# Optimization experiments

Hardware: AMD Instinct MI355X
Metric: run time of the kernel (lower is better)

## Reference

```python
import jax, jax.numpy as jnp
import numpy as np

B, L, E, HL, HS, V, NC = 64, 512, 512, 1024, 256, 32000, 5
TAU = 1.0


def setup_inputs() -> dict:
    key = jax.random.key(0)
    ks = jax.random.split(key, 17)
    def p(k, shape, s=0.08):
        return jax.random.normal(k, shape, dtype=jnp.float32) * s
    eps = 1e-6
    return {
        "x": jax.random.randint(ks[0], (B, L), 0, V, dtype=jnp.int32),
        "gumbel_u": jax.random.uniform(ks[1], (B, L, 2), dtype=jnp.float32, minval=eps, maxval=1.0 - eps),
        "embedding": p(ks[2], (V, E), 0.1),
        "W_ih_l": p(ks[3], (4 * HL, E)),
        "W_hh_l": p(ks[4], (4 * HL, HL)),
        "b_ih_l": p(ks[5], (4 * HL,)),
        "b_hh_l": p(ks[6], (4 * HL,)),
        "W_ih_s": p(ks[7], (4 * HS, E)),
        "W_hh_s": p(ks[8], (4 * HS, HS)),
        "b_ih_s": p(ks[9], (4 * HS,)),
        "b_hh_s": p(ks[10], (4 * HS,)),
        "W_p": p(ks[11], (2, E + 2 * HL)),
        "b_p": p(ks[12], (2,)),
        "W_c1": p(ks[13], (512, HL)),
        "b_c1": p(ks[14], (512,)),
        "W_c2": p(ks[15], (NC, 512)),
        "b_c2": p(ks[16], (NC,)),
    }


def _lstm_cell(x, h, c, Wih, Whh, bih, bhh):
    # torch.nn.LSTMCell gate order: i, f, g, o
    gates = x @ Wih.T + bih + h @ Whh.T + bhh
    i, f, g, o = jnp.split(gates, 4, axis=-1)
    c2 = jax.nn.sigmoid(f) * c + jax.nn.sigmoid(i) * jnp.tanh(g)
    h2 = jax.nn.sigmoid(o) * jnp.tanh(c2)
    return h2, c2


def _forward(x, gumbel_u, embedding, W_ih_l, W_hh_l, b_ih_l, b_hh_l,
             W_ih_s, W_hh_s, b_ih_s, b_hh_s, W_p, b_p, W_c1, b_c1, W_c2, b_c2):
    emb = embedding[x]                       # [B, L, E]
    xs = (jnp.swapaxes(emb, 0, 1),           # [L, B, E]
          jnp.swapaxes(gumbel_u, 0, 1))      # [L, B, 2]
    dt = embedding.dtype
    init = (jnp.zeros((B, HL), dt), jnp.zeros((B, HL), dt),
            jnp.zeros((B, HS), dt), jnp.zeros((B, HS), dt))

    def step(carry, xs_t):
        h_l, c_l, h_s, c_s = carry
        e_t, u_t = xs_t
        h_l_new, c_l_new = _lstm_cell(e_t, h_l, c_l, W_ih_l, W_hh_l, b_ih_l, b_hh_l)
        h_s_new, c_s_new = _lstm_cell(e_t, h_s, c_s, W_ih_s, W_hh_s, b_ih_s, b_hh_s)
        p_t = jnp.concatenate([e_t, h_l_new, c_l_new], axis=1) @ W_p.T + b_p  # [B, 2]
        # training-mode gumbel: r = softmax(-log(-log(u)) / tau); note p_t is NOT used (faithful)
        g = -jnp.log(-jnp.log(u_t))
        r = jax.nn.softmax(g / TAU, axis=-1)  # [B, 2]
        # skim branch: small h over first HS dims, tail from previous large h / new large c
        h_blend = jnp.concatenate([h_s_new, h_l[:, HS:]], axis=1)
        c_blend = jnp.concatenate([c_s_new, c_l_new[:, HS:]], axis=1)
        h_next = r[:, :1] * h_l_new + r[:, 1:] * h_blend
        c_next = r[:, :1] * c_l_new + r[:, 1:] * c_blend
        return (h_next, c_next, h_s_new, c_s_new), (h_next, p_t)

    (h_l, c_l, h_s, c_s), (h_seq, p_seq) = jax.lax.scan(step, init, xs)
    h_stack = jnp.swapaxes(h_seq, 0, 1)                       # [B, L, HL]
    p_stack = jax.nn.softmax(jnp.swapaxes(p_seq, 0, 1), -1)   # [B, L, 2]
    z = jax.nn.relu(h_l) @ W_c1.T + b_c1
    z = jax.nn.relu(z)  # dropout is identity in eval
    logits = jax.nn.softmax(z @ W_c2.T + b_c2, axis=-1)       # [B, NC]
    return logits, h_stack, p_stack


def reference(x, gumbel_u, embedding, W_ih_l, W_hh_l, b_ih_l, b_hh_l,
              W_ih_s, W_hh_s, b_ih_s, b_hh_s, W_p, b_p, W_c1, b_c1, W_c2, b_c2):
    return _forward(x, gumbel_u, embedding, W_ih_l, W_hh_l, b_ih_l, b_hh_l,
                    W_ih_s, W_hh_s, b_ih_s, b_hh_s, W_p, b_p, W_c1, b_c1, W_c2, b_c2)
```

## Files before the change

### kernel.cpp

```cpp
#include <hip/hip_runtime.h>
#include <stdint.h>
#include <stddef.h>

#define B_   64
#define L_   512
#define E_   512
#define HL_  1024
#define HS_  256
#define NC_  5
#define KL_  (E_ + HL_)
#define KS_  (E_ + HS_)
#define ROWS_L_ 4096
#define ROWS_S_ 1024
#define ROWS_TOT_ 5120
#define SL_  8
#define SS_  4

typedef __attribute__((ext_vector_type(8))) short bf16x8;
typedef __attribute__((ext_vector_type(4))) float f32x4;

__device__ __forceinline__ uint16_t f2bf(float f) {
  union { float f; uint32_t u; } v; v.f = f;
  uint32_t r = v.u + 0x7FFFu + ((v.u >> 16) & 1u);
  return (uint16_t)(r >> 16);
}
__device__ __forceinline__ float bf2f(uint16_t h) {
  union { uint32_t u; float f; } v; v.u = ((uint32_t)h) << 16; return v.f;
}
__device__ __forceinline__ float sigm(float x) { return 1.0f / (1.0f + expf(-x)); }


__global__ __launch_bounds__(256) void k_convw(
    const float* __restrict__ Wihl, const float* __restrict__ Whhl,
    const float* __restrict__ Wihs, const float* __restrict__ Whhs,
    uint16_t* __restrict__ Wl_hi, uint16_t* __restrict__ Wl_lo,
    uint16_t* __restrict__ Ws_hi, uint16_t* __restrict__ Ws_lo) {
  const int N1 = ROWS_L_ * KL_;
  const int N2 = ROWS_S_ * KS_;
  int idx = blockIdx.x * 256 + threadIdx.x;
  if (idx < N1) {
    int row = idx / KL_, k = idx - row * KL_;
    float v = (k < E_) ? Wihl[row * E_ + k] : Whhl[row * HL_ + (k - E_)];
    uint16_t hi = f2bf(v);
    Wl_hi[idx] = hi;
    Wl_lo[idx] = f2bf(v - bf2f(hi));
  } else if (idx < N1 + N2) {
    int j = idx - N1;
    int row = j / KS_, k = j - row * KS_;
    float v = (k < E_) ? Wihs[row * E_ + k] : Whhs[row * HS_ + (k - E_)];
    uint16_t hi = f2bf(v);
    Ws_hi[j] = hi;
    Ws_lo[j] = f2bf(v - bf2f(hi));
  }
}

__global__ __launch_bounds__(256) void k_embed(
    const int* __restrict__ x, const float* __restrict__ emb,
    uint16_t* __restrict__ Ahi, uint16_t* __restrict__ Alo) {
  int idx = blockIdx.x * 256 + threadIdx.x;
  int t = idx >> 15;
  int rem = idx & 32767;
  int b = rem >> 9;
  int k = rem & 511;
  int tok = x[b * L_ + t];
  float v = emb[(size_t)tok * E_ + k];
  uint16_t hi = f2bf(v);
  Ahi[idx] = hi;
  Alo[idx] = f2bf(v - bf2f(hi));
}

__global__ __launch_bounds__(256) void k_zero(uint32_t* __restrict__ p, int nwords) {
  int idx = blockIdx.x * 256 + threadIdx.x;
  if (idx < nwords) p[idx] = 0u;
}

__global__ __launch_bounds__(256) void k_rseq(
    const float* __restrict__ gum, float* __restrict__ rseq) {
  int idx = blockIdx.x * 256 + threadIdx.x;
  int t = idx >> 6, b = idx & 63;
  float u0 = gum[(b * L_ + t) * 2 + 0];
  float u1 = gum[(b * L_ + t) * 2 + 1];
  float g0 = -logf(-logf(u0));
  float g1 = -logf(-logf(u1));
  float m = fmaxf(g0, g1);
  float e0 = expf(g0 - m), e1 = expf(g1 - m);
  float inv = 1.0f / (e0 + e1);
  rseq[idx * 2 + 0] = e0 * inv;
  rseq[idx * 2 + 1] = e1 * inv;
}

__global__ __launch_bounds__(256) void k_pe(
    const int* __restrict__ x, const float* __restrict__ emb,
    const float* __restrict__ Wp, float* __restrict__ Pe) {
  int idx = blockIdx.x * 256 + threadIdx.x;
  int t = idx >> 6, b = idx & 63;
  int tok = x[b * L_ + t];
  const float* row = emb + (size_t)tok * E_;
  float a0 = 0.f, a1 = 0.f;
  for (int k = 0; k < E_; ++k) {
    float e = row[k];
    a0 += e * Wp[k];
    a1 += e * Wp[(E_ + 2 * HL_) + k];
  }
  Pe[idx * 2 + 0] = a0;
  Pe[idx * 2 + 1] = a1;
}

__global__ __launch_bounds__(64) void k_step_gemm(
    const uint16_t* __restrict__ Ahi, const uint16_t* __restrict__ Alo,
    const uint16_t* __restrict__ h_hi, const uint16_t* __restrict__ h_lo,
    const uint16_t* __restrict__ hs_hi, const uint16_t* __restrict__ hs_lo,
    const uint16_t* __restrict__ Wl_hi, const uint16_t* __restrict__ Wl_lo,
    const uint16_t* __restrict__ Ws_hi, const uint16_t* __restrict__ Ws_lo,
    float* __restrict__ partial, int t) {
  int bid = blockIdx.x;
  int lane = threadIdx.x;
  int quad = lane >> 4, l16 = lane & 15;
  const uint16_t* actE_hi = Ahi + (size_t)t * (B_ * E_);
  const uint16_t* actE_lo = Alo + (size_t)t * (B_ * E_);
  const uint16_t *actH_hi, *actH_lo, *W_hi, *W_lo;
  int r0, s, wstride, hstride, rbase;
  if (bid < 512) {
    int rt = bid >> 3; s = bid & 7;
    r0 = rt * 64; W_hi = Wl_hi; W_lo = Wl_lo; wstride = KL_;
    actH_hi = h_hi; actH_lo = h_lo; hstride = HL_; rbase = 0;
  } else {
    int b2 = bid - 512;
    int rt = b2 >> 2; s = b2 & 3;
    r0 = rt * 64; W_hi = Ws_hi; W_lo = Ws_lo; wstride = KS_;
    actH_hi = hs_hi; actH_lo = hs_lo; hstride = HS_; rbase = ROWS_L_;
  }
  int k0 = s * 192;

  f32x4 acc[4][4];
#pragma unroll
  for (int mt = 0; mt < 4; ++mt)
#pragma unroll
    for (int nt = 0; nt < 4; ++nt) {
      acc[mt][nt][0] = 0.f; acc[mt][nt][1] = 0.f;
      acc[mt][nt][2] = 0.f; acc[mt][nt][3] = 0.f;
    }

  int ko = quad * 8;
#pragma unroll
  for (int kk = 0; kk < 6; ++kk) {
    int kbase = k0 + kk * 32;
    bf16x8 a_hi[4], a_lo[4], b_hi[4], b_lo[4];
#pragma unroll
    for (int mt = 0; mt < 4; ++mt) {
      int m = mt * 16 + l16;
      const uint16_t* phi;
      const uint16_t* plo;
      if (kbase < E_) {
        phi = actE_hi + m * E_ + kbase;
        plo = actE_lo + m * E_ + kbase;
      } else {
        phi = actH_hi + m * hstride + (kbase - E_);
        plo = actH_lo + m * hstride + (kbase - E_);
      }
      a_hi[mt] = *reinterpret_cast<const bf16x8*>(phi + ko);
      a_lo[mt] = *reinterpret_cast<const bf16x8*>(plo + ko);
    }
#pragma unroll
    for (int nt = 0; nt < 4; ++nt) {
      int n = r0 + nt * 16 + l16;
      b_hi[nt] = *reinterpret_cast<const bf16x8*>(W_hi + (size_t)n * wstride + kbase + ko);
      b_lo[nt] = *reinterpret_cast<const bf16x8*>(W_lo + (size_t)n * wstride + kbase + ko);
    }
#pragma unroll
    for (int mt = 0; mt < 4; ++mt)
#pragma unroll
      for (int nt = 0; nt < 4; ++nt) {
        acc[mt][nt] = __builtin_amdgcn_mfma_f32_16x16x32_bf16(a_hi[mt], b_hi[nt], acc[mt][nt], 0, 0, 0);
        acc[mt][nt] = __builtin_amdgcn_mfma_f32_16x16x32_bf16(a_lo[mt], b_hi[nt], acc[mt][nt], 0, 0, 0);
        acc[mt][nt] = __builtin_amdgcn_mfma_f32_16x16x32_bf16(a_hi[mt], b_lo[nt], acc[mt][nt], 0, 0, 0);
      }
  }

#pragma unroll
  for (int mt = 0; mt < 4; ++mt)
#pragma unroll
    for (int nt = 0; nt < 4; ++nt)
#pragma unroll
      for (int r = 0; r < 4; ++r) {
        int b = mt * 16 + quad * 4 + r;
        int row = rbase + r0 + nt * 16 + l16;
        partial[((size_t)s * B_ + b) * ROWS_TOT_ + row] = acc[mt][nt][r];
      }
}

__global__ __launch_bounds__(256) void k_step_point(
    const float* __restrict__ partial, float* __restrict__ c_l,
    float* __restrict__ h_f, uint16_t* __restrict__ h_hi, uint16_t* __restrict__ h_lo,
    float* __restrict__ c_s, uint16_t* __restrict__ hs_hi, uint16_t* __restrict__ hs_lo,
    float* __restrict__ p_acc, const float* __restrict__ rseq,
    const float* __restrict__ bihl, const float* __restrict__ bhhl,
    const float* __restrict__ bihs, const float* __restrict__ bhhs,
    const float* __restrict__ Wp, float* __restrict__ out_h, int t) {
  int bb = blockIdx.x >> 2, cc = blockIdx.x & 3;
  int tid = threadIdx.x;
  int d = cc * 256 + tid;

  float g4[4];
#pragma unroll
  for (int g = 0; g < 4; ++g) {
    int row = g * HL_ + d;
    float v = bihl[row] + bhhl[row];
#pragma unroll
    for (int s = 0; s < SL_; ++s)
      v += partial[((size_t)s * B_ + bb) * ROWS_TOT_ + row];
    g4[g] = v;
  }
  float cprev = c_l[bb * HL_ + d];
  float cn = sigm(g4[1]) * cprev + sigm(g4[0]) * tanhf(g4[2]);
  float hn = sigm(g4[3]) * tanhf(cn);

  float hs_new = 0.f, cs_new = 0.f;
  if (cc == 0) {
    float gs[4];
#pragma unroll
    for (int g = 0; g < 4; ++g) {
      int row = ROWS_L_ + g * HS_ + d;
      float v = bihs[g * HS_ + d] + bhhs[g * HS_ + d];
#pragma unroll
      for (int s = 0; s < SS_; ++s)
        v += partial[((size_t)s * B_ + bb) * ROWS_TOT_ + row];
      gs[g] = v;
    }
    float csp = c_s[bb * HS_ + d];
    cs_new = sigm(gs[1]) * csp + sigm(gs[0]) * tanhf(gs[2]);
    hs_new = sigm(gs[3]) * tanhf(cs_new);
    c_s[bb * HS_ + d] = cs_new;
    uint16_t hi = f2bf(hs_new);
    hs_hi[bb * HS_ + d] = hi;
    hs_lo[bb * HS_ + d] = f2bf(hs_new - bf2f(hi));
  }

  float r0v = rseq[(t * B_ + bb) * 2 + 0];
  float r1v = rseq[(t * B_ + bb) * 2 + 1];
  float hb = (cc == 0) ? hs_new : h_f[bb * HL_ + d];
  float cb = (cc == 0) ? cs_new : cn;
  float hnext = r0v * hn + r1v * hb;
  float cnext = r0v * cn + r1v * cb;

  c_l[bb * HL_ + d] = cnext;
  h_f[bb * HL_ + d] = hnext;
  uint16_t hhi = f2bf(hnext);
  h_hi[bb * HL_ + d] = hhi;
  h_lo[bb * HL_ + d] = f2bf(hnext - bf2f(hhi));
  out_h[((size_t)bb * L_ + t) * HL_ + d] = hnext;

  float p0 = hn * Wp[E_ + d] + cn * Wp[E_ + HL_ + d];
  float p1 = hn * Wp[(E_ + 2 * HL_) + E_ + d] + cn * Wp[(E_ + 2 * HL_) + E_ + HL_ + d];
  __shared__ float s0[256], s1[256];
  s0[tid] = p0; s1[tid] = p1;
  __syncthreads();
  for (int off = 128; off > 0; off >>= 1) {
    if (tid < off) { s0[tid] += s0[tid + off]; s1[tid] += s1[tid + off]; }
    __syncthreads();
  }
  if (tid == 0) {
    atomicAdd(&p_acc[(t * B_ + bb) * 2 + 0], s0[0]);
    atomicAdd(&p_acc[(t * B_ + bb) * 2 + 1], s1[0]);
  }
}


__global__ __launch_bounds__(256) void k_cls1(
    const float* __restrict__ h_f, const float* __restrict__ Wc1,
    const float* __restrict__ bc1, float* __restrict__ z1) {
  int idx = blockIdx.x * 256 + threadIdx.x;
  int b = idx >> 9, j = idx & 511;
  float s = bc1[j];
  const float* hr = h_f + b * HL_;
  const float* wr = Wc1 + (size_t)j * HL_;
  for (int d = 0; d < HL_; ++d) s += fmaxf(hr[d], 0.f) * wr[d];
  z1[idx] = fmaxf(s, 0.f);
}

__global__ __launch_bounds__(64) void k_cls2(
    const float* __restrict__ z1, const float* __restrict__ Wc2,
    const float* __restrict__ bc2, float* __restrict__ out) {
  int b = blockIdx.x;
  int tid = threadIdx.x;
  __shared__ float sv[NC_];
  if (tid < NC_) {
    float s = bc2[tid];
    const float* zr = z1 + b * 512;
    const float* wr = Wc2 + tid * 512;
    for (int k = 0; k < 512; ++k) s += zr[k] * wr[k];
    sv[tid] = s;
  }
  __syncthreads();
  if (tid == 0) {
    float m = sv[0];
    for (int j = 1; j < NC_; ++j) m = fmaxf(m, sv[j]);
    float e[NC_], sum = 0.f;
    for (int j = 0; j < NC_; ++j) { e[j] = expf(sv[j] - m); sum += e[j]; }
    float inv = 1.0f / sum;
    for (int j = 0; j < NC_; ++j) out[b * NC_ + j] = e[j] * inv;
  }
}

__global__ __launch_bounds__(256) void k_pfinal(
    const float* __restrict__ p_acc, const float* __restrict__ Pe,
    const float* __restrict__ bp, float* __restrict__ out_p) {
  int idx = blockIdx.x * 256 + threadIdx.x;
  int b = idx >> 9, t = idx & 511;
  int i2 = (t * B_ + b) * 2;
  float v0 = p_acc[i2 + 0] + Pe[i2 + 0] + bp[0];
  float v1 = p_acc[i2 + 1] + Pe[i2 + 1] + bp[1];
  float m = fmaxf(v0, v1);
  float e0 = expf(v0 - m), e1 = expf(v1 - m);
  float inv = 1.0f / (e0 + e1);
  out_p[(size_t)idx * 2 + 0] = e0 * inv;
  out_p[(size_t)idx * 2 + 1] = e1 * inv;
}

extern "C" void kernel_launch(void* const* d_in, const int* in_sizes, int n_in,
                              void* d_out, int out_size, void* d_ws, size_t ws_size,
                              hipStream_t stream) {
  const int*   x    = (const int*)d_in[0];
  const float* gum  = (const float*)d_in[1];
  const float* emb  = (const float*)d_in[2];
  const float* Wihl = (const float*)d_in[3];
  const float* Whhl = (const float*)d_in[4];
  const float* bihl = (const float*)d_in[5];
  const float* bhhl = (const float*)d_in[6];
  const float* Wihs = (const float*)d_in[7];
  const float* Whhs = (const float*)d_in[8];
  const float* bihs = (const float*)d_in[9];
  const float* bhhs = (const float*)d_in[10];
  const float* Wp   = (const float*)d_in[11];
  const float* bp   = (const float*)d_in[12];
  const float* Wc1  = (const float*)d_in[13];
  const float* bc1  = (const float*)d_in[14];
  const float* Wc2  = (const float*)d_in[15];
  const float* bc2  = (const float*)d_in[16];
  float* out = (float*)d_out;

  char* ws = (char*)d_ws;
  uint16_t* Ahi   = (uint16_t*)(ws + 0);
  uint16_t* Alo   = (uint16_t*)(ws + 33554432);
  uint16_t* Wl_hi = (uint16_t*)(ws + 67108864);
  uint16_t* Wl_lo = (uint16_t*)(ws + 79691776);
  uint16_t* Ws_hi = (uint16_t*)(ws + 92274688);
  uint16_t* Ws_lo = (uint16_t*)(ws + 93847552);
  float*    part  = (float*)   (ws + 95420416);
  float*    c_l   = (float*)   (ws + 105906176);
  float*    h_f   = (float*)   (ws + 106168320);
  float*    c_s   = (float*)   (ws + 106430464);
  float*    p_acc = (float*)   (ws + 106496000);
  uint16_t* h_hi  = (uint16_t*)(ws + 106758144);
  uint16_t* h_lo  = (uint16_t*)(ws + 106889216);
  uint16_t* hs_hi = (uint16_t*)(ws + 107020288);
  uint16_t* hs_lo = (uint16_t*)(ws + 107053056);
  float*    Pe    = (float*)   (ws + 107085824);
  float*    rseq  = (float*)   (ws + 107347968);
  float*    z1    = (float*)   (ws + 107610112);

  float* out_logits = out;
  float* out_h      = out + 320;
  float* out_p      = out + 320 + (size_t)B_ * L_ * HL_;

  {
    int n = ROWS_L_ * KL_ + ROWS_S_ * KS_;
    k_convw<<<(n + 255) / 256, 256, 0, stream>>>(Wihl, Whhl, Wihs, Whhs,
                                                 Wl_hi, Wl_lo, Ws_hi, Ws_lo);
  }
  k_embed<<<(L_ * B_ * E_) / 256, 256, 0, stream>>>(x, emb, Ahi, Alo);
  {
    int nwords = (107085824 - 105906176) / 4;
    k_zero<<<(nwords + 255) / 256, 256, 0, stream>>>((uint32_t*)(ws + 105906176), nwords);
  }
  k_rseq<<<(L_ * B_) / 256, 256, 0, stream>>>(gum, rseq);
  k_pe<<<(L_ * B_) / 256, 256, 0, stream>>>(x, emb, Wp, Pe);

  for (int t = 0; t < L_; ++t) {
    k_step_gemm<<<576, 64, 0, stream>>>(Ahi, Alo, h_hi, h_lo, hs_hi, hs_lo,
                                        Wl_hi, Wl_lo, Ws_hi, Ws_lo, part, t);
    k_step_point<<<256, 256, 0, stream>>>(part, c_l, h_f, h_hi, h_lo, c_s, hs_hi, hs_lo,
                                          p_acc, rseq, bihl, bhhl, bihs, bhhs,
                                          Wp, out_h, t);
  }

  k_cls1<<<(B_ * 512) / 256, 256, 0, stream>>>(h_f, Wc1, bc1, z1);
  k_cls2<<<B_, 64, 0, stream>>>(z1, Wc2, bc2, out_logits);
  k_pfinal<<<(B_ * L_) / 256, 256, 0, stream>>>(p_acc, Pe, bp, out_p);
}
```

Baseline: 10.68 ms.

## Replace per-step kernel launches with a persistent cooperative scan kernel

Replaces the 1024 per-timestep launches (a GEMM kernel plus a pointwise kernel) with one persistent cooperative kernel. Each workgroup keeps its slice of the hi/lo bf16 LSTM weights in registers, reduces split-K partials in shared memory, applies the cell update in place, and synchronises through grid.sync once per step. The small-LSTM workgroups run one step ahead of the large-LSTM ones so the skim state is ready when the blend needs it. The embedding low-order correction term is dropped, which lowers precision of the input projection, and the p-logit atomics become per-workgroup partials reduced in a final kernel.

```diff
diff --git a/kernel.cpp b/kernel.cpp
--- a/kernel.cpp
+++ b/kernel.cpp
@@ -1,6 +1,9 @@
 #include <hip/hip_runtime.h>
+#include <hip/hip_cooperative_groups.h>
 #include <stdint.h>
 #include <stddef.h>
+
+namespace cg = cooperative_groups;
 
 #define B_   64
 #define L_   512
@@ -8,13 +11,10 @@
 #define HL_  1024
 #define HS_  256
 #define NC_  5
-#define KL_  (E_ + HL_)
-#define KS_  (E_ + HS_)
-#define ROWS_L_ 4096
-#define ROWS_S_ 1024
-#define ROWS_TOT_ 5120
-#define SL_  8
-#define SS_  4
+#define KL_  1536
+#define KS_  768
+#define NWG_L 128
+#define NWG_  160
 
 typedef __attribute__((ext_vector_type(8))) short bf16x8;
 typedef __attribute__((ext_vector_type(4))) float f32x4;
@@ -35,8 +35,8 @@
     const float* __restrict__ Wihs, const float* __restrict__ Whhs,
     uint16_t* __restrict__ Wl_hi, uint16_t* __restrict__ Wl_lo,
     uint16_t* __restrict__ Ws_hi, uint16_t* __restrict__ Ws_lo) {
-  const int N1 = ROWS_L_ * KL_;
-  const int N2 = ROWS_S_ * KS_;
+  const int N1 = 4096 * KL_;
+  const int N2 = 1024 * KS_;
   int idx = blockIdx.x * 256 + threadIdx.x;
   if (idx < N1) {
     int row = idx / KL_, k = idx - row * KL_;
@@ -56,17 +56,14 @@
 
 __global__ __launch_bounds__(256) void k_embed(
     const int* __restrict__ x, const float* __restrict__ emb,
-    uint16_t* __restrict__ Ahi, uint16_t* __restrict__ Alo) {
+    uint16_t* __restrict__ Ahi) {
   int idx = blockIdx.x * 256 + threadIdx.x;
   int t = idx >> 15;
   int rem = idx & 32767;
   int b = rem >> 9;
   int k = rem & 511;
   int tok = x[b * L_ + t];
-  float v = emb[(size_t)tok * E_ + k];
-  uint16_t hi = f2bf(v);
-  Ahi[idx] = hi;
-  Alo[idx] = f2bf(v - bf2f(hi));
+  Ahi[idx] = f2bf(emb[(size_t)tok * E_ + k]);
 }
 
 __global__ __launch_bounds__(256) void k_zero(uint32_t* __restrict__ p, int nwords) {
@@ -100,181 +97,266 @@
   for (int k = 0; k < E_; ++k) {
     float e = row[k];
     a0 += e * Wp[k];
-    a1 += e * Wp[(E_ + 2 * HL_) + k];
+    a1 += e * Wp[2560 + k];
   }
   Pe[idx * 2 + 0] = a0;
   Pe[idx * 2 + 1] = a1;
 }
 
-__global__ __launch_bounds__(64) void k_step_gemm(
-    const uint16_t* __restrict__ Ahi, const uint16_t* __restrict__ Alo,
-    const uint16_t* __restrict__ h_hi, const uint16_t* __restrict__ h_lo,
-    const uint16_t* __restrict__ hs_hi, const uint16_t* __restrict__ hs_lo,
-    const uint16_t* __restrict__ Wl_hi, const uint16_t* __restrict__ Wl_lo,
-    const uint16_t* __restrict__ Ws_hi, const uint16_t* __restrict__ Ws_lo,
-    float* __restrict__ partial, int t) {
-  int bid = blockIdx.x;
-  int lane = threadIdx.x;
-  int quad = lane >> 4, l16 = lane & 15;
-  const uint16_t* actE_hi = Ahi + (size_t)t * (B_ * E_);
-  const uint16_t* actE_lo = Alo + (size_t)t * (B_ * E_);
-  const uint16_t *actH_hi, *actH_lo, *W_hi, *W_lo;
-  int r0, s, wstride, hstride, rbase;
-  if (bid < 512) {
-    int rt = bid >> 3; s = bid & 7;
-    r0 = rt * 64; W_hi = Wl_hi; W_lo = Wl_lo; wstride = KL_;
-    actH_hi = h_hi; actH_lo = h_lo; hstride = HL_; rbase = 0;
+struct ScanArgs {
+  const uint16_t* Ahi;
+  const uint16_t* Wl_hi; const uint16_t* Wl_lo;
+  const uint16_t* Ws_hi; const uint16_t* Ws_lo;
+  uint16_t* h_hi; uint16_t* h_lo;
+  uint16_t* hs_hi; uint16_t* hs_lo;
+  float* hs_f32; float* cs_f32;
+  const float* rseq;
+  const float* bihl; const float* bhhl;
+  const float* bihs; const float* bhhs;
+  const float* Wp;
+  float* out_h; float* pPart;
+};
+
+__global__ __launch_bounds__(512, 2) void k_scan(ScanArgs A) {
+  cg::grid_group grid = cg::this_grid();
+  const int w    = blockIdx.x;
+  const int tid  = threadIdx.x;
+  const int lane = tid & 63;
+  const int ws   = tid >> 6;
+  const int l16  = lane & 15;
+  const int quad = lane >> 4;
+  const int pj   = tid & 7;
+  const int pb   = tid >> 3;
+  const bool isL = (w < NWG_L);
+
+  __shared__ float par[8][32][68];
+  __shared__ float pbuf[64][17];
+
+  bf16x8 bwh[2][6], bwl[2][6];
+  if (isL) {
+#pragma unroll
+    for (int nt = 0; nt < 2; ++nt) {
+      int nl = nt * 16 + l16;
+      int g = nl >> 3, j = nl & 7;
+      const size_t roff = (size_t)(g * HL_ + 8 * w + j) * KL_;
+#pragma unroll
+      for (int kt = 0; kt < 6; ++kt) {
+        int k = ws * 32 + kt * 256 + quad * 8;
+        bwh[nt][kt] = *reinterpret_cast<const bf16x8*>(A.Wl_hi + roff + k);
+        bwl[nt][kt] = *reinterpret_cast<const bf16x8*>(A.Wl_lo + roff + k);
+      }
+    }
   } else {
-    int b2 = bid - 512;
-    int rt = b2 >> 2; s = b2 & 3;
-    r0 = rt * 64; W_hi = Ws_hi; W_lo = Ws_lo; wstride = KS_;
-    actH_hi = hs_hi; actH_lo = hs_lo; hstride = HS_; rbase = ROWS_L_;
-  }
-  int k0 = s * 192;
-
-  f32x4 acc[4][4];
-#pragma unroll
-  for (int mt = 0; mt < 4; ++mt)
-#pragma unroll
-    for (int nt = 0; nt < 4; ++nt) {
-      acc[mt][nt][0] = 0.f; acc[mt][nt][1] = 0.f;
-      acc[mt][nt][2] = 0.f; acc[mt][nt][3] = 0.f;
+    int w2 = w - NWG_L;
+#pragma unroll
+    for (int nt = 0; nt < 2; ++nt) {
+      int nl = nt * 16 + l16;
+      int g = nl >> 3, j = nl & 7;
+      const size_t roff = (size_t)(g * HS_ + 8 * w2 + j) * KS_;
+#pragma unroll
+      for (int kt = 0; kt < 3; ++kt) {
+        int k = ws * 32 + kt * 256 + quad * 8;
+        bwh[nt][kt] = *reinterpret_cast<const bf16x8*>(A.Ws_hi + roff + k);
+        bwl[nt][kt] = *reinterpret_cast<const bf16x8*>(A.Ws_lo + roff + k);
+      }
     }
-
-  int ko = quad * 8;
-#pragma unroll
-  for (int kk = 0; kk < 6; ++kk) {
-    int kbase = k0 + kk * 32;
-    bf16x8 a_hi[4], a_lo[4], b_hi[4], b_lo[4];
-#pragma unroll
-    for (int mt = 0; mt < 4; ++mt) {
-      int m = mt * 16 + l16;
-      const uint16_t* phi;
-      const uint16_t* plo;
-      if (kbase < E_) {
-        phi = actE_hi + m * E_ + kbase;
-        plo = actE_lo + m * E_ + kbase;
-      } else {
-        phi = actH_hi + m * hstride + (kbase - E_);
-        plo = actH_lo + m * hstride + (kbase - E_);
+  }
+
+  float c_st = 0.f, h_st = 0.f;
+
+  float b4[4];
+  float wph0 = 0.f, wpc0 = 0.f, wph1 = 0.f, wpc1 = 0.f;
+  int d;
+  if (isL) {
+    d = 8 * w + pj;
+#pragma unroll
+    for (int g = 0; g < 4; ++g) b4[g] = A.bihl[g * HL_ + d] + A.bhhl[g * HL_ + d];
+    wph0 = A.Wp[E_ + d];        wpc0 = A.Wp[E_ + HL_ + d];
+    wph1 = A.Wp[2560 + E_ + d]; wpc1 = A.Wp[2560 + E_ + HL_ + d];
+  } else {
+    d = 8 * (w - NWG_L) + pj;
+#pragma unroll
+    for (int g = 0; g < 4; ++g) b4[g] = A.bihs[g * HS_ + d] + A.bhhs[g * HS_ + d];
+  }
+
+#pragma unroll 1
+  for (int it = -1; it < L_; ++it) {
+    if (isL) {
+      if (it >= 0) {
+        const int t = it;
+        f32x4 acc[4][2];
+#pragma unroll
+        for (int mt = 0; mt < 4; ++mt)
+#pragma unroll
+          for (int nt = 0; nt < 2; ++nt) {
+            acc[mt][nt][0] = 0.f; acc[mt][nt][1] = 0.f;
+            acc[mt][nt][2] = 0.f; acc[mt][nt][3] = 0.f;
+          }
+        const uint16_t* eh = A.Ahi + (size_t)t * (B_ * E_);
+        const uint16_t* hh = A.h_hi + ((t - 1) & 1) * (B_ * HL_);
+        const uint16_t* hl = A.h_lo + ((t - 1) & 1) * (B_ * HL_);
+#pragma unroll
+        for (int kt = 0; kt < 2; ++kt) {
+          const int koff = ws * 32 + kt * 256 + quad * 8;
+          bf16x8 ah[4];
+#pragma unroll
+          for (int mt = 0; mt < 4; ++mt)
+            ah[mt] = *reinterpret_cast<const bf16x8*>(eh + (mt * 16 + l16) * E_ + koff);
+#pragma unroll
+          for (int mt = 0; mt < 4; ++mt)
+#pragma unroll
+            for (int nt = 0; nt < 2; ++nt) {
+              acc[mt][nt] = __builtin_amdgcn_mfma_f32_16x16x32_bf16(ah[mt], bwh[nt][kt], acc[mt][nt], 0, 0, 0);
+              acc[mt][nt] = __builtin_amdgcn_mfma_f32_16x16x32_bf16(ah[mt], bwl[nt][kt], acc[mt][nt], 0, 0, 0);
+            }
+        }
+#pragma unroll
+        for (int kt = 2; kt < 6; ++kt) {
+          const int koff = ws * 32 + (kt - 2) * 256 + quad * 8;
+          bf16x8 ah[4], al[4];
+#pragma unroll
+          for (int mt = 0; mt < 4; ++mt) {
+            ah[mt] = *reinterpret_cast<const bf16x8*>(hh + (mt * 16 + l16) * HL_ + koff);
+            al[mt] = *reinterpret_cast<const bf16x8*>(hl + (mt * 16 + l16) * HL_ + koff);
+          }
+#pragma unroll
+          for (int mt = 0; mt < 4; ++mt)
+#pragma unroll
+            for (int nt = 0; nt < 2; ++nt) {
+              acc[mt][nt] = __builtin_amdgcn_mfma_f32_16x16x32_bf16(ah[mt], bwh[nt][kt], acc[mt][nt], 0, 0, 0);
+              acc[mt][nt] = __builtin_amdgcn_mfma_f32_16x16x32_bf16(al[mt], bwh[nt][kt], acc[mt][nt], 0, 0, 0);
+              acc[mt][nt] = __builtin_amdgcn_mfma_f32_16x16x32_bf16(ah[mt], bwl[nt][kt], acc[mt][nt], 0, 0, 0);
+            }
+        }
+#pragma unroll
+        for (int mt = 0; mt < 4; ++mt)
+#pragma unroll
+          for (int nt = 0; nt < 2; ++nt)
+            *reinterpret_cast<f32x4*>(&par[ws][nt * 16 + l16][mt * 16 + quad * 4]) = acc[mt][nt];
+        __syncthreads();
+        float g4[4];
+#pragma unroll
+        for (int g = 0; g < 4; ++g) {
+          float v = b4[g];
+#pragma unroll
+          for (int s = 0; s < 8; ++s) v += par[s][g * 8 + pj][pb];
+          g4[g] = v;
+        }
+        float cn = sigm(g4[1]) * c_st + sigm(g4[0]) * tanhf(g4[2]);
+        float hn = sigm(g4[3]) * tanhf(cn);
+        float r0 = A.rseq[(t * B_ + pb) * 2 + 0];
+        float r1 = A.rseq[(t * B_ + pb) * 2 + 1];
+        float hb, cb2;
+        if (d < HS_) {
+          hb  = A.hs_f32[(t & 1) * (B_ * HS_) + pb * HS_ + d];
+          cb2 = A.cs_f32[(t & 1) * (B_ * HS_) + pb * HS_ + d];
+        } else {
+          hb = h_st; cb2 = cn;
+        }
+        float hnext = r0 * hn + r1 * hb;
+        float cnext = r0 * cn + r1 * cb2;
+        c_st = cnext; h_st = hnext;
+        uint16_t hhi16 = f2bf(hnext);
+        A.h_hi[(t & 1) * (B_ * HL_) + pb * HL_ + d] = hhi16;
+        A.h_lo[(t & 1) * (B_ * HL_) + pb * HL_ + d] = f2bf(hnext - bf2f(hhi16));
+        A.out_h[((size_t)pb * L_ + t) * HL_ + d] = hnext;
+        pbuf[pb][pj * 2 + 0] = hn * wph0 + cn * wpc0;
+        pbuf[pb][pj * 2 + 1] = hn * wph1 + cn * wpc1;
+        __syncthreads();
+        if (tid < 128) {
+          int b = tid >> 1, c = tid & 1;
+          float s = 0.f;
+#pragma unroll
+          for (int j = 0; j < 8; ++j) s += pbuf[b][j * 2 + c];
+          A.pPart[(((size_t)t * NWG_L + w) * B_ + b) * 2 + c] = s;
+        }
       }
-      a_hi[mt] = *reinterpret_cast<const bf16x8*>(phi + ko);
-      a_lo[mt] = *reinterpret_cast<const bf16x8*>(plo + ko);
+    } else {
+      const int ts = it + 1;
+      if (ts < L_) {
+        f32x4 acc[4][2];
+#pragma unroll
+        for (int mt = 0; mt < 4; ++mt)
+#pragma unroll
+          for (int nt = 0; nt < 2; ++nt) {
+            acc[mt][nt][0] = 0.f; acc[mt][nt][1] = 0.f;
+            acc[mt][nt][2] = 0.f; acc[mt][nt][3] = 0.f;
+          }
+        const uint16_t* eh = A.Ahi + (size_t)ts * (B_ * E_);
+        const uint16_t* hh = A.hs_hi + ((ts - 1) & 1) * (B_ * HS_);
+        const uint16_t* hl = A.hs_lo + ((ts - 1) & 1) * (B_ * HS_);
+#pragma unroll
+        for (int kt = 0; kt < 2; ++kt) {
+          const int koff = ws * 32 + kt * 256 + quad * 8;
+          bf16x8 ah[4];
+#pragma unroll
+          for (int mt = 0; mt < 4; ++mt)
+            ah[mt] = *reinterpret_cast<const bf16x8*>(eh + (mt * 16 + l16) * E_ + koff);
+#pragma unroll
+          for (int mt = 0; mt < 4; ++mt)
+#pragma unroll
+            for (int nt = 0; nt < 2; ++nt) {
+              acc[mt][nt] = __builtin_amdgcn_mfma_f32_16x16x32_bf16(ah[mt], bwh[nt][kt], acc[mt][nt], 0, 0, 0);
+              acc[mt][nt] = __builtin_amdgcn_mfma_f32_16x16x32_bf16(ah[mt], bwl[nt][kt], acc[mt][nt], 0, 0, 0);
+            }
+        }
+        {
+          const int koff = ws * 32 + quad * 8;
+          bf16x8 ah[4], al[4];
+#pragma unroll
+          for (int mt = 0; mt < 4; ++mt) {
+            ah[mt] = *reinterpret_cast<const bf16x8*>(hh + (mt * 16 + l16) * HS_ + koff);
+            al[mt] = *reinterpret_cast<const bf16x8*>(hl + (mt * 16 + l16) * HS_ + koff);
+          }
+#pragma unroll
+          for (int mt = 0; mt < 4; ++mt)
+#pragma unroll
+            for (int nt = 0; nt < 2; ++nt) {
+              acc[mt][nt] = __builtin_amdgcn_mfma_f32_16x16x32_bf16(ah[mt], bwh[nt][2], acc[mt][nt], 0, 0, 0);
+              acc[mt][nt] = __builtin_amdgcn_mfma_f32_16x16x32_bf16(al[mt], bwh[nt][2], acc[mt][nt], 0, 0, 0);
+              acc[mt][nt] = __builtin_amdgcn_mfma_f32_16x16x32_bf16(ah[mt], bwl[nt][2], acc[mt][nt], 0, 0, 0);
+            }
+        }
+#pragma unroll
+        for (int mt = 0; mt < 4; ++mt)
+#pragma unroll
+          for (int nt = 0; nt < 2; ++nt)
+            *reinterpret_cast<f32x4*>(&par[ws][nt * 16 + l16][mt * 16 + quad * 4]) = acc[mt][nt];
+        __syncthreads();
+        float g4[4];
+#pragma unroll
+        for (int g = 0; g < 4; ++g) {
+          float v = b4[g];
+#pragma unroll
+          for (int s = 0; s < 8; ++s) v += par[s][g * 8 + pj][pb];
+          g4[g] = v;
+        }
+        float csn = sigm(g4[1]) * c_st + sigm(g4[0]) * tanhf(g4[2]);
+        float hsn = sigm(g4[3]) * tanhf(csn);
+        c_st = csn;
+        int o = (ts & 1) * (B_ * HS_) + pb * HS_ + d;
+        uint16_t hh16 = f2bf(hsn);
+        A.hs_hi[o] = hh16;
+        A.hs_lo[o] = f2bf(hsn - bf2f(hh16));
+        A.hs_f32[o] = hsn;
+        A.cs_f32[o] = csn;
+        __syncthreads();
+      }
     }
-#pragma unroll
-    for (int nt = 0; nt < 4; ++nt) {
-      int n = r0 + nt * 16 + l16;
-      b_hi[nt] = *reinterpret_cast<const bf16x8*>(W_hi + (size_t)n * wstride + kbase + ko);
-      b_lo[nt] = *reinterpret_cast<const bf16x8*>(W_lo + (size_t)n * wstride + kbase + ko);
-    }
-#pragma unroll
-    for (int mt = 0; mt < 4; ++mt)
-#pragma unroll
-      for (int nt = 0; nt < 4; ++nt) {
-        acc[mt][nt] = __builtin_amdgcn_mfma_f32_16x16x32_bf16(a_hi[mt], b_hi[nt], acc[mt][nt], 0, 0, 0);
-        acc[mt][nt] = __builtin_amdgcn_mfma_f32_16x16x32_bf16(a_lo[mt], b_hi[nt], acc[mt][nt], 0, 0, 0);
-        acc[mt][nt] = __builtin_amdgcn_mfma_f32_16x16x32_bf16(a_hi[mt], b_lo[nt], acc[mt][nt], 0, 0, 0);
-      }
-  }
-
-#pragma unroll
-  for (int mt = 0; mt < 4; ++mt)
-#pragma unroll
-    for (int nt = 0; nt < 4; ++nt)
-#pragma unroll
-      for (int r = 0; r < 4; ++r) {
-        int b = mt * 16 + quad * 4 + r;
-        int row = rbase + r0 + nt * 16 + l16;
-        partial[((size_t)s * B_ + b) * ROWS_TOT_ + row] = acc[mt][nt][r];
-      }
-}
-
-__global__ __launch_bounds__(256) void k_step_point(
-    const float* __restrict__ partial, float* __restrict__ c_l,
-    float* __restrict__ h_f, uint16_t* __restrict__ h_hi, uint16_t* __restrict__ h_lo,
-    float* __restrict__ c_s, uint16_t* __restrict__ hs_hi, uint16_t* __restrict__ hs_lo,
-    float* __restrict__ p_acc, const float* __restrict__ rseq,
-    const float* __restrict__ bihl, const float* __restrict__ bhhl,
-    const float* __restrict__ bihs, const float* __restrict__ bhhs,
-    const float* __restrict__ Wp, float* __restrict__ out_h, int t) {
-  int bb = blockIdx.x >> 2, cc = blockIdx.x & 3;
-  int tid = threadIdx.x;
-  int d = cc * 256 + tid;
-
-  float g4[4];
-#pragma unroll
-  for (int g = 0; g < 4; ++g) {
-    int row = g * HL_ + d;
-    float v = bihl[row] + bhhl[row];
-#pragma unroll
-    for (int s = 0; s < SL_; ++s)
-      v += partial[((size_t)s * B_ + bb) * ROWS_TOT_ + row];
-    g4[g] = v;
-  }
-  float cprev = c_l[bb * HL_ + d];
-  float cn = sigm(g4[1]) * cprev + sigm(g4[0]) * tanhf(g4[2]);
-  float hn = sigm(g4[3]) * tanhf(cn);
-
-  float hs_new = 0.f, cs_new = 0.f;
-  if (cc == 0) {
-    float gs[4];
-#pragma unroll
-    for (int g = 0; g < 4; ++g) {
-      int row = ROWS_L_ + g * HS_ + d;
-      float v = bihs[g * HS_ + d] + bhhs[g * HS_ + d];
-#pragma unroll
-      for (int s = 0; s < SS_; ++s)
-        v += partial[((size_t)s * B_ + bb) * ROWS_TOT_ + row];
-      gs[g] = v;
-    }
-    float csp = c_s[bb * HS_ + d];
-    cs_new = sigm(gs[1]) * csp + sigm(gs[0]) * tanhf(gs[2]);
-    hs_new = sigm(gs[3]) * tanhf(cs_new);
-    c_s[bb * HS_ + d] = cs_new;
-    uint16_t hi = f2bf(hs_new);
-    hs_hi[bb * HS_ + d] = hi;
-    hs_lo[bb * HS_ + d] = f2bf(hs_new - bf2f(hi));
-  }
-
-  float r0v = rseq[(t * B_ + bb) * 2 + 0];
-  float r1v = rseq[(t * B_ + bb) * 2 + 1];
-  float hb = (cc == 0) ? hs_new : h_f[bb * HL_ + d];
-  float cb = (cc == 0) ? cs_new : cn;
-  float hnext = r0v * hn + r1v * hb;
-  float cnext = r0v * cn + r1v * cb;
-
-  c_l[bb * HL_ + d] = cnext;
-  h_f[bb * HL_ + d] = hnext;
-  uint16_t hhi = f2bf(hnext);
-  h_hi[bb * HL_ + d] = hhi;
-  h_lo[bb * HL_ + d] = f2bf(hnext - bf2f(hhi));
-  out_h[((size_t)bb * L_ + t) * HL_ + d] = hnext;
-
-  float p0 = hn * Wp[E_ + d] + cn * Wp[E_ + HL_ + d];
-  float p1 = hn * Wp[(E_ + 2 * HL_) + E_ + d] + cn * Wp[(E_ + 2 * HL_) + E_ + HL_ + d];
-  __shared__ float s0[256], s1[256];
-  s0[tid] = p0; s1[tid] = p1;
-  __syncthreads();
-  for (int off = 128; off > 0; off >>= 1) {
-    if (tid < off) { s0[tid] += s0[tid + off]; s1[tid] += s1[tid + off]; }
-    __syncthreads();
-  }
-  if (tid == 0) {
-    atomicAdd(&p_acc[(t * B_ + bb) * 2 + 0], s0[0]);
-    atomicAdd(&p_acc[(t * B_ + bb) * 2 + 1], s1[0]);
+    grid.sync();
   }
 }
 
 
 __global__ __launch_bounds__(256) void k_cls1(
-    const float* __restrict__ h_f, const float* __restrict__ Wc1,
+    const float* __restrict__ out_h, const float* __restrict__ Wc1,
     const float* __restrict__ bc1, float* __restrict__ z1) {
   int idx = blockIdx.x * 256 + threadIdx.x;
   int b = idx >> 9, j = idx & 511;
   float s = bc1[j];
-  const float* hr = h_f + b * HL_;
+  const float* hr = out_h + (size_t)b * L_ * HL_ + (size_t)(L_ - 1) * HL_;
   const float* wr = Wc1 + (size_t)j * HL_;
-  for (int d = 0; d < HL_; ++d) s += fmaxf(hr[d], 0.f) * wr[d];
+  for (int dd = 0; dd < HL_; ++dd) s += fmaxf(hr[dd], 0.f) * wr[dd];
   z1[idx] = fmaxf(s, 0.f);
 }
 
@@ -303,15 +385,19 @@
 }
 
 __global__ __launch_bounds__(256) void k_pfinal(
-    const float* __restrict__ p_acc, const float* __restrict__ Pe,
+    const float* __restrict__ pPart, const float* __restrict__ Pe,
     const float* __restrict__ bp, float* __restrict__ out_p) {
   int idx = blockIdx.x * 256 + threadIdx.x;
   int b = idx >> 9, t = idx & 511;
-  int i2 = (t * B_ + b) * 2;
-  float v0 = p_acc[i2 + 0] + Pe[i2 + 0] + bp[0];
-  float v1 = p_acc[i2 + 1] + Pe[i2 + 1] + bp[1];
-  float m = fmaxf(v0, v1);
-  float e0 = expf(v0 - m), e1 = expf(v1 - m);
+  float s0 = Pe[(t * B_ + b) * 2 + 0] + bp[0];
+  float s1 = Pe[(t * B_ + b) * 2 + 1] + bp[1];
+  for (int w = 0; w < NWG_L; ++w) {
+    const float* p = pPart + (((size_t)t * NWG_L + w) * B_ + b) * 2;
+    s0 += p[0];
+    s1 += p[1];
+  }
+  float m = fmaxf(s0, s1);
+  float e0 = expf(s0 - m), e1 = expf(s1 - m);
   float inv = 1.0f / (e0 + e1);
   out_p[(size_t)idx * 2 + 0] = e0 * inv;
   out_p[(size_t)idx * 2 + 1] = e1 * inv;
@@ -341,50 +427,48 @@
 
   char* ws = (char*)d_ws;
   uint16_t* Ahi   = (uint16_t*)(ws + 0);
-  uint16_t* Alo   = (uint16_t*)(ws + 33554432);
-  uint16_t* Wl_hi = (uint16_t*)(ws + 67108864);
-  uint16_t* Wl_lo = (uint16_t*)(ws + 79691776);
-  uint16_t* Ws_hi = (uint16_t*)(ws + 92274688);
-  uint16_t* Ws_lo = (uint16_t*)(ws + 93847552);
-  float*    part  = (float*)   (ws + 95420416);
-  float*    c_l   = (float*)   (ws + 105906176);
-  float*    h_f   = (float*)   (ws + 106168320);
-  float*    c_s   = (float*)   (ws + 106430464);
-  float*    p_acc = (float*)   (ws + 106496000);
-  uint16_t* h_hi  = (uint16_t*)(ws + 106758144);
-  uint16_t* h_lo  = (uint16_t*)(ws + 106889216);
-  uint16_t* hs_hi = (uint16_t*)(ws + 107020288);
-  uint16_t* hs_lo = (uint16_t*)(ws + 107053056);
-  float*    Pe    = (float*)   (ws + 107085824);
-  float*    rseq  = (float*)   (ws + 107347968);
-  float*    z1    = (float*)   (ws + 107610112);
+  uint16_t* Wl_hi = (uint16_t*)(ws + 33554432);
+  uint16_t* Wl_lo = (uint16_t*)(ws + 46137344);
+  uint16_t* Ws_hi = (uint16_t*)(ws + 58720256);
+  uint16_t* Ws_lo = (uint16_t*)(ws + 60293120);
+  float*    pPart = (float*)   (ws + 61865984);
+  uint16_t* h_hi  = (uint16_t*)(ws + 95420416);
+  uint16_t* h_lo  = (uint16_t*)(ws + 95682560);
+  uint16_t* hs_hi = (uint16_t*)(ws + 95944704);
+  uint16_t* hs_lo = (uint16_t*)(ws + 96010240);
+  float*    hs_f  = (float*)   (ws + 96075776);
+  float*    cs_f  = (float*)   (ws + 96206848);
+  float*    rseq  = (float*)   (ws + 96337920);
+  float*    Pe    = (float*)   (ws + 96600064);
+  float*    z1    = (float*)   (ws + 96862208);
 
   float* out_logits = out;
   float* out_h      = out + 320;
   float* out_p      = out + 320 + (size_t)B_ * L_ * HL_;
 
   {
-    int n = ROWS_L_ * KL_ + ROWS_S_ * KS_;
+    int n = 4096 * KL_ + 1024 * KS_;
     k_convw<<<(n + 255) / 256, 256, 0, stream>>>(Wihl, Whhl, Wihs, Whhs,
                                                  Wl_hi, Wl_lo, Ws_hi, Ws_lo);
   }
-  k_embed<<<(L_ * B_ * E_) / 256, 256, 0, stream>>>(x, emb, Ahi, Alo);
+  k_embed<<<(L_ * B_ * E_) / 256, 256, 0, stream>>>(x, emb, Ahi);
   {
-    int nwords = (107085824 - 105906176) / 4;
-    k_zero<<<(nwords + 255) / 256, 256, 0, stream>>>((uint32_t*)(ws + 105906176), nwords);
+    int nwords = (96337920 - 95420416) / 4;
+    k_zero<<<(nwords + 255) / 256, 256, 0, stream>>>((uint32_t*)(ws + 95420416), nwords);
   }
   k_rseq<<<(L_ * B_) / 256, 256, 0, stream>>>(gum, rseq);
   k_pe<<<(L_ * B_) / 256, 256, 0, stream>>>(x, emb, Wp, Pe);
 
-  for (int t = 0; t < L_; ++t) {
-    k_step_gemm<<<576, 64, 0, stream>>>(Ahi, Alo, h_hi, h_lo, hs_hi, hs_lo,
-                                        Wl_hi, Wl_lo, Ws_hi, Ws_lo, part, t);
-    k_step_point<<<256, 256, 0, stream>>>(part, c_l, h_f, h_hi, h_lo, c_s, hs_hi, hs_lo,
-                                          p_acc, rseq, bihl, bhhl, bihs, bhhs,
-                                          Wp, out_h, t);
-  }
-
-  k_cls1<<<(B_ * 512) / 256, 256, 0, stream>>>(h_f, Wc1, bc1, z1);
+  ScanArgs sa;
+  sa.Ahi = Ahi; sa.Wl_hi = Wl_hi; sa.Wl_lo = Wl_lo; sa.Ws_hi = Ws_hi; sa.Ws_lo = Ws_lo;
+  sa.h_hi = h_hi; sa.h_lo = h_lo; sa.hs_hi = hs_hi; sa.hs_lo = hs_lo;
+  sa.hs_f32 = hs_f; sa.cs_f32 = cs_f;
+  sa.rseq = rseq; sa.bihl = bihl; sa.bhhl = bhhl; sa.bihs = bihs; sa.bhhs = bhhs;
+  sa.Wp = Wp; sa.out_h = out_h; sa.pPart = pPart;
+  void* args[] = { &sa };
+  hipLaunchCooperativeKernel((const void*)k_scan, dim3(NWG_), dim3(512), args, 0, stream);
+
+  k_cls1<<<(B_ * 512) / 256, 256, 0, stream>>>(out_h, Wc1, bc1, z1);
   k_cls2<<<B_, 64, 0, stream>>>(z1, Wc2, bc2, out_logits);
-  k_pfinal<<<(B_ * L_) / 256, 256, 0, stream>>>(p_acc, Pe, bp, out_p);
-}
+  k_pfinal<<<(B_ * L_) / 256, 256, 0, stream>>>(pPart, Pe, bp, out_p);
+}
```

Result: slower. 15.90 ms (+48.8%).
